# Kernel tuning notes

Hardware: AMD Instinct MI355X
Metric: run time of the kernel (lower is better)

The kernel has to match this reference:

```python
import jax, jax.numpy as jnp
import numpy as np

def setup_inputs() -> dict:
    key = jax.random.key(0)
    k1, k2, k3 = jax.random.split(key, 3)
    shape = (2, 2048, 8, 64)  # [n, l, h, d]
    return {
        "q": jax.random.normal(k1, shape, dtype=jnp.float32),
        "k": jax.random.normal(k2, shape, dtype=jnp.float32),
        "v": jax.random.normal(k3, shape, dtype=jnp.float32),
    }

def reference(q, k, v):
    # QK^T: [n, l, s, h]
    qk = jnp.einsum('nlhd,nshd->nlsh', q, k)
    softmax_temp = 1.0 / (q.shape[3] ** 0.5)
    attn = jax.nn.softmax(softmax_temp * qk, axis=2)
    # weighted values: [n, l, h, d]
    return jnp.einsum('nlsh,nshd->nlhd', attn, v)
```

## Files before the change

kernel.cpp:

```cpp
#include <hip/hip_runtime.h>
#include <hip/hip_bf16.h>
#include <math.h>

typedef float floatx16 __attribute__((ext_vector_type(16)));
typedef __bf16 bf16x8 __attribute__((ext_vector_type(8)));

#define SEQ 2048
#define NH 8
#define DH 64
#define HEADS 16
#define HSTRIDE (SEQ * DH)
#define TILE_E (64 * 64)
#define SLOT_B 32768

__device__ __forceinline__ unsigned short f2bf(float x) {
  union { __bf16 b; unsigned short u; } c; c.b = (__bf16)x; return c.u;
}
__device__ __forceinline__ unsigned int pk2bf(float a, float b) {
  union { __hip_bfloat162 h2; unsigned int u; } c;
  c.h2 = __float22bfloat162_rn(make_float2(a, b));
  return c.u;
}

__device__ __forceinline__ void hswap_fwd(unsigned& a, unsigned& b) {
  asm volatile("v_permlane32_swap_b32 %0, %1" : "+v"(a), "+v"(b));
}
__device__ __forceinline__ void hswap_rev(unsigned& a, unsigned& b) {
  asm volatile("v_permlane32_swap_b32 %0, %1" : "+v"(b), "+v"(a));
}

__device__ __forceinline__ void lds_dma16(const void* g, void* l) {
  __builtin_amdgcn_global_load_lds(
      (const __attribute__((address_space(1))) void*)g,
      (__attribute__((address_space(3))) void*)l, 16, 0, 0);
}

__global__ __launch_bounds__(256)
void pack_kv(const float* __restrict__ k, const float* __restrict__ v,
             unsigned short* __restrict__ kb, unsigned short* __restrict__ vb) {
  __shared__ unsigned short Ts[64][68];
  const int tid  = threadIdx.x;
  const int bx   = blockIdx.x;
  const int head = bx & 15;
  const int kt   = bx >> 4;
  const int n = head >> 3, h = head & 7;

  #pragma unroll
  for (int j2 = 0; j2 < 2; ++j2) {
    int c = j2 * 256 + tid;
    int lane = c & 63;
    int kk = (c >> 6) & 3, ks2 = c >> 8;
    int row = kt * 64 + ks2 * 32 + (lane & 31);
    int d0  = kk * 16 + (lane >> 5) * 8;
    const float* src = k + ((size_t)(n * SEQ + row) * NH + h) * DH + d0;
    float4 a = *(const float4*)src;
    float4 b = *(const float4*)(src + 4);
    ushort4 lo, hi;
    lo.x = f2bf(a.x); lo.y = f2bf(a.y); lo.z = f2bf(a.z); lo.w = f2bf(a.w);
    hi.x = f2bf(b.x); hi.y = f2bf(b.y); hi.z = f2bf(b.z); hi.w = f2bf(b.w);
    unsigned short* dst = kb + (size_t)head * HSTRIDE + kt * TILE_E + c * 8;
    *(ushort4*)dst = lo;
    *(ushort4*)(dst + 4) = hi;
  }

  #pragma unroll
  for (int i = 0; i < 4; ++i) {
    int id = i * 256 + tid;
    int s  = id >> 4;
    int c4 = (id & 15) * 4;
    size_t g = ((size_t)((n * SEQ + kt * 64 + s) * NH + h)) * DH + c4;
    float4 x = *(const float4*)(v + g);
    ushort4 y;
    y.x = f2bf(x.x); y.y = f2bf(x.y); y.z = f2bf(x.z); y.w = f2bf(x.w);
    *(ushort4*)&Ts[s][c4] = y;
  }
  __syncthreads();
  #pragma unroll
  for (int j2 = 0; j2 < 2; ++j2) {
    int c = j2 * 256 + tid;
    int lane = c & 63;
    int dsub = (c >> 6) & 1, ss = c >> 7;
    int s0 = ss * 16 + (lane >> 5) * 8;
    int d  = dsub * 32 + (lane & 31);
    ushort4 lo, hi;
    lo.x = Ts[s0 + 0][d]; lo.y = Ts[s0 + 1][d]; lo.z = Ts[s0 + 2][d]; lo.w = Ts[s0 + 3][d];
    hi.x = Ts[s0 + 4][d]; hi.y = Ts[s0 + 5][d]; hi.z = Ts[s0 + 6][d]; hi.w = Ts[s0 + 7][d];
    unsigned short* dst = vb + (size_t)head * HSTRIDE + kt * TILE_E + c * 8;
    *(ushort4*)dst = lo;
    *(ushort4*)(dst + 4) = hi;
  }
}

__global__ __launch_bounds__(256)
void attn(const float* __restrict__ q, const unsigned short* __restrict__ kb,
          const unsigned short* __restrict__ vt, float* __restrict__ out) {
  __shared__ __align__(16) char lds[2 * SLOT_B];
  float* oM = (float*)lds;
  float* lM = (float*)(lds + 4 * 16 * 72 * 4);

  const int tid  = threadIdx.x;
  const int wave = tid >> 6;
  const int lane = tid & 63;
  const int l32  = lane & 31;
  const int hl   = lane >> 5;
  const int wq   = wave >> 1;
  const int wk   = wave & 1;

  unsigned px = (unsigned)lane, py = (unsigned)lane + 100u;
  hswap_fwd(px, py);
  const bool mir = (__builtin_amdgcn_readfirstlane(px) != 0u);

  const int bx   = blockIdx.x;
  const int head = bx & 15;
  const int qc   = bx >> 4;
  const int n = head >> 3, h = head & 7;

  const unsigned short* kf = kb + (size_t)head * HSTRIDE;
  const unsigned short* vf = vt + (size_t)head * HSTRIDE;

  auto stage = [&](int i, int slot) {
    const unsigned short* g = ((wave & 1) ? vf : kf)
                            + (size_t)((wave >> 1) * 16 + i) * TILE_E;
    char* lb = lds + slot * SLOT_B + wave * 8192;
    #pragma unroll
    for (int j = 0; j < 8; ++j)
      lds_dma16(g + (j * 64 + lane) * 8, lb + j * 1024);
  };

  const float S = 0.125f * 1.4426950408889634f;

  bf16x8 qB[4];
  #pragma unroll
  for (int kk = 0; kk < 4; ++kk) {
    const int row = qc * 64 + wq * 32 + l32;
    const float* src = q + ((size_t)((n * SEQ + row) * NH + h)) * DH + kk * 16 + hl * 8;
    float4 x0 = *(const float4*)src;
    float4 x1 = *(const float4*)(src + 4);
    union { unsigned int u32[4]; bf16x8 v8; } u;
    u.u32[0] = pk2bf(x0.x * S, x0.y * S); u.u32[1] = pk2bf(x0.z * S, x0.w * S);
    u.u32[2] = pk2bf(x1.x * S, x1.y * S); u.u32[3] = pk2bf(x1.z * S, x1.w * S);
    qB[kk] = u.v8;
  }

  floatx16 o[2];
  float lsum = 0.f;
  #pragma unroll
  for (int d = 0; d < 2; ++d)
    #pragma unroll
    for (int i = 0; i < 16; ++i) o[d][i] = 0.f;

  stage(0, 0);

  for (int it = 0; it < 16; ++it) {
    asm volatile("s_waitcnt vmcnt(0)" ::: "memory");
    __builtin_amdgcn_s_barrier();
    __builtin_amdgcn_sched_barrier(0);
    if (it < 15) stage(it + 1, (it + 1) & 1);

    const char* tb = lds + (it & 1) * SLOT_B + wk * 16384;

    bf16x8 kA0[4], kA1[4];
    bf16x8 vb0[2][2], vb1[2][2];
    #pragma unroll
    for (int kk = 0; kk < 4; ++kk)
      kA0[kk] = *(const bf16x8*)(tb + (kk * 64 + lane) * 16);
    #pragma unroll
    for (int kk = 0; kk < 4; ++kk)
      kA1[kk] = *(const bf16x8*)(tb + ((4 + kk) * 64 + lane) * 16);
    #pragma unroll
    for (int j = 0; j < 2; ++j)
      #pragma unroll
      for (int d = 0; d < 2; ++d) {
        vb0[j][d] = *(const bf16x8*)(tb + 8192 + ((j * 2 + d) * 64 + lane) * 16);
        vb1[j][d] = *(const bf16x8*)(tb + 8192 + (((2 + j) * 2 + d) * 64 + lane) * 16);
      }

    floatx16 acc0;
    #pragma unroll
    for (int i = 0; i < 16; ++i) acc0[i] = 0.f;
    __builtin_amdgcn_s_setprio(1);
    #pragma unroll
    for (int kk = 0; kk < 4; ++kk)
      acc0 = __builtin_amdgcn_mfma_f32_32x32x16_bf16(kA0[kk], qB[kk], acc0, 0, 0, 0);
    __builtin_amdgcn_s_setprio(0);

    unsigned pkv0[8];
    #pragma unroll
    for (int g2 = 0; g2 < 4; ++g2) {
      float p0 = __builtin_amdgcn_exp2f(acc0[4 * g2 + 0]);
      float p1 = __builtin_amdgcn_exp2f(acc0[4 * g2 + 1]);
      float p2 = __builtin_amdgcn_exp2f(acc0[4 * g2 + 2]);
      float p3 = __builtin_amdgcn_exp2f(acc0[4 * g2 + 3]);
      lsum += (p0 + p1) + (p2 + p3);
      pkv0[g2 * 2]     = pk2bf(p0, p1);
      pkv0[g2 * 2 + 1] = pk2bf(p2, p3);
    }

    floatx16 acc1;
    #pragma unroll
    for (int i = 0; i < 16; ++i) acc1[i] = 0.f;
    __builtin_amdgcn_s_setprio(1);
    #pragma unroll
    for (int kk = 0; kk < 4; ++kk)
      acc1 = __builtin_amdgcn_mfma_f32_32x32x16_bf16(kA1[kk], qB[kk], acc1, 0, 0, 0);
    __builtin_amdgcn_s_setprio(0);

    {
      union { unsigned u32[4]; bf16x8 v8; } A1, A2;
      A1.u32[0] = pkv0[0]; A1.u32[2] = pkv0[2];
      A1.u32[1] = pkv0[1]; A1.u32[3] = pkv0[3];
      A2.u32[0] = pkv0[4]; A2.u32[2] = pkv0[6];
      A2.u32[1] = pkv0[5]; A2.u32[3] = pkv0[7];
      if (!mir) {
        hswap_fwd(A1.u32[0], A1.u32[2]); hswap_fwd(A1.u32[1], A1.u32[3]);
        hswap_fwd(A2.u32[0], A2.u32[2]); hswap_fwd(A2.u32[1], A2.u32[3]);
      } else {
        hswap_rev(A1.u32[0], A1.u32[2]); hswap_rev(A1.u32[1], A1.u32[3]);
        hswap_rev(A2.u32[0], A2.u32[2]); hswap_rev(A2.u32[1], A2.u32[3]);
      }
      __builtin_amdgcn_s_setprio(1);
      o[0] = __builtin_amdgcn_mfma_f32_32x32x16_bf16(A1.v8, vb0[0][0], o[0], 0, 0, 0);
      o[1] = __builtin_amdgcn_mfma_f32_32x32x16_bf16(A1.v8, vb0[0][1], o[1], 0, 0, 0);
      o[0] = __builtin_amdgcn_mfma_f32_32x32x16_bf16(A2.v8, vb0[1][0], o[0], 0, 0, 0);
      o[1] = __builtin_amdgcn_mfma_f32_32x32x16_bf16(A2.v8, vb0[1][1], o[1], 0, 0, 0);
      __builtin_amdgcn_s_setprio(0);
    }

    {
      unsigned pkv1[8];
      #pragma unroll
      for (int g2 = 0; g2 < 4; ++g2) {
        float p0 = __builtin_amdgcn_exp2f(acc1[4 * g2 + 0]);
        float p1 = __builtin_amdgcn_exp2f(acc1[4 * g2 + 1]);
        float p2 = __builtin_amdgcn_exp2f(acc1[4 * g2 + 2]);
        float p3 = __builtin_amdgcn_exp2f(acc1[4 * g2 + 3]);
        lsum += (p0 + p1) + (p2 + p3);
        pkv1[g2 * 2]     = pk2bf(p0, p1);
        pkv1[g2 * 2 + 1] = pk2bf(p2, p3);
      }
      union { unsigned u32[4]; bf16x8 v8; } A1, A2;
      A1.u32[0] = pkv1[0]; A1.u32[2] = pkv1[2];
      A1.u32[1] = pkv1[1]; A1.u32[3] = pkv1[3];
      A2.u32[0] = pkv1[4]; A2.u32[2] = pkv1[6];
      A2.u32[1] = pkv1[5]; A2.u32[3] = pkv1[7];
      if (!mir) {
        hswap_fwd(A1.u32[0], A1.u32[2]); hswap_fwd(A1.u32[1], A1.u32[3]);
        hswap_fwd(A2.u32[0], A2.u32[2]); hswap_fwd(A2.u32[1], A2.u32[3]);
      } else {
        hswap_rev(A1.u32[0], A1.u32[2]); hswap_rev(A1.u32[1], A1.u32[3]);
        hswap_rev(A2.u32[0], A2.u32[2]); hswap_rev(A2.u32[1], A2.u32[3]);
      }
      __builtin_amdgcn_s_setprio(1);
      o[0] = __builtin_amdgcn_mfma_f32_32x32x16_bf16(A1.v8, vb1[0][0], o[0], 0, 0, 0);
      o[1] = __builtin_amdgcn_mfma_f32_32x32x16_bf16(A1.v8, vb1[0][1], o[1], 0, 0, 0);
      o[0] = __builtin_amdgcn_mfma_f32_32x32x16_bf16(A2.v8, vb1[1][0], o[0], 0, 0, 0);
      o[1] = __builtin_amdgcn_mfma_f32_32x32x16_bf16(A2.v8, vb1[1][1], o[1], 0, 0, 0);
      __builtin_amdgcn_s_setprio(0);
    }
  }

  lsum += __shfl_xor(lsum, 32, 64);

  const int prow = tid >> 4;
  const int col4 = tid & 15;
  #pragma unroll
  for (int p = 0; p < 4; ++p) {
    const int qsel = p >> 1, rh = p & 1;
    __syncthreads();
    #pragma unroll
    for (int r8 = 0; r8 < 8; ++r8) {
      const int r   = rh * 8 + r8;
      const int rip = (r8 & 3) + 4 * hl + 8 * (r8 >> 2);
      oM[(wave * 16 + rip) * 72 + l32]      = o[0][r];
      oM[(wave * 16 + rip) * 72 + 32 + l32] = o[1][r];
    }
    if (lane < 32 && ((lane >> 4) & 1) == rh) lM[wave * 16 + (lane & 15)] = lsum;
    __syncthreads();
    float4 s = make_float4(0.f, 0.f, 0.f, 0.f);
    float l = 0.f;
    #pragma unroll
    for (int j = 0; j < 2; ++j) {
      const int w = qsel * 2 + j;
      float4 t4 = *(const float4*)&oM[(w * 16 + prow) * 72 + col4 * 4];
      s.x += t4.x; s.y += t4.y; s.z += t4.z; s.w += t4.w;
      l += lM[w * 16 + prow];
    }
    float inv = 1.f / l;
    const int grow = qc * 64 + qsel * 32 + rh * 16 + prow;
    float4 st; st.x = s.x * inv; st.y = s.y * inv; st.z = s.z * inv; st.w = s.w * inv;
    *(float4*)(out + ((size_t)((n * SEQ + grow) * NH + h)) * DH + col4 * 4) = st;
  }
}

extern "C" void kernel_launch(void* const* d_in, const int* in_sizes, int n_in,
                              void* d_out, int out_size, void* d_ws, size_t ws_size,
                              hipStream_t stream) {
  const float* q = (const float*)d_in[0];
  const float* k = (const float*)d_in[1];
  const float* v = (const float*)d_in[2];
  float* out = (float*)d_out;
  (void)in_sizes; (void)n_in; (void)out_size; (void)ws_size;

  unsigned short* kb = (unsigned short*)d_ws;
  unsigned short* vb = kb + (size_t)HEADS * HSTRIDE;

  pack_kv<<<HEADS * (SEQ / 64), 256, 0, stream>>>(k, v, kb, vb);
  attn<<<HEADS * (SEQ / 64), 256, 0, stream>>>(q, kb, vb, out);
}
```

Before: 102.4 us.

## Use 512-thread blocks with 128 query rows and triple-buffered KV staging

```diff
diff --git a/kernel.cpp b/kernel.cpp
--- a/kernel.cpp
+++ b/kernel.cpp
@@ -12,6 +12,7 @@
 #define HSTRIDE (SEQ * DH)
 #define TILE_E (64 * 64)
 #define SLOT_B 32768
+#define NSLOT 3
 
 __device__ __forceinline__ unsigned short f2bf(float x) {
   union { __bf16 b; unsigned short u; } c; c.b = (__bf16)x; return c.u;
@@ -91,12 +92,12 @@
   }
 }
 
-__global__ __launch_bounds__(256)
+__global__ __launch_bounds__(512)
 void attn(const float* __restrict__ q, const unsigned short* __restrict__ kb,
           const unsigned short* __restrict__ vt, float* __restrict__ out) {
-  __shared__ __align__(16) char lds[2 * SLOT_B];
+  extern __shared__ __align__(16) char lds[];
   float* oM = (float*)lds;
-  float* lM = (float*)(lds + 4 * 16 * 72 * 4);
+  float* lM = (float*)(lds + 8 * 16 * 72 * 4);
 
   const int tid  = threadIdx.x;
   const int wave = tid >> 6;
@@ -112,19 +113,23 @@
 
   const int bx   = blockIdx.x;
   const int head = bx & 15;
-  const int qc   = bx >> 4;
+  const int qb   = bx >> 4;
   const int n = head >> 3, h = head & 7;
 
   const unsigned short* kf = kb + (size_t)head * HSTRIDE;
   const unsigned short* vf = vt + (size_t)head * HSTRIDE;
 
   auto stage = [&](int i, int slot) {
-    const unsigned short* g = ((wave & 1) ? vf : kf)
-                            + (size_t)((wave >> 1) * 16 + i) * TILE_E;
-    char* lb = lds + slot * SLOT_B + wave * 8192;
-    #pragma unroll
-    for (int j = 0; j < 8; ++j)
-      lds_dma16(g + (j * 64 + lane) * 8, lb + j * 1024);
+    const int tsel  = wave >> 2;
+    const int kvsel = (wave >> 1) & 1;
+    const int half  = wave & 1;
+    const unsigned short* g = (kvsel ? vf : kf) + (size_t)(tsel * 16 + i) * TILE_E;
+    char* lb = lds + slot * SLOT_B + tsel * 16384 + kvsel * 8192 + half * 4096;
+    #pragma unroll
+    for (int j = 0; j < 4; ++j) {
+      const int frag = half * 4 + j;
+      lds_dma16(g + (frag * 64 + lane) * 8, lb + j * 1024);
+    }
   };
 
   const float S = 0.125f * 1.4426950408889634f;
@@ -132,7 +137,7 @@
   bf16x8 qB[4];
   #pragma unroll
   for (int kk = 0; kk < 4; ++kk) {
-    const int row = qc * 64 + wq * 32 + l32;
+    const int row = qb * 128 + wq * 32 + l32;
     const float* src = q + ((size_t)((n * SEQ + row) * NH + h)) * DH + kk * 16 + hl * 8;
     float4 x0 = *(const float4*)src;
     float4 x1 = *(const float4*)(src + 4);
@@ -149,15 +154,23 @@
     #pragma unroll
     for (int i = 0; i < 16; ++i) o[d][i] = 0.f;
 
+  asm volatile("s_waitcnt vmcnt(0)" ::: "memory");
+  __builtin_amdgcn_sched_barrier(0);
+
   stage(0, 0);
+  stage(1, 1);
 
   for (int it = 0; it < 16; ++it) {
-    asm volatile("s_waitcnt vmcnt(0)" ::: "memory");
+    if (it < 15) asm volatile("s_waitcnt vmcnt(4)" ::: "memory");
+    else         asm volatile("s_waitcnt vmcnt(0)" ::: "memory");
     __builtin_amdgcn_s_barrier();
     __builtin_amdgcn_sched_barrier(0);
-    if (it < 15) stage(it + 1, (it + 1) & 1);
-
-    const char* tb = lds + (it & 1) * SLOT_B + wk * 16384;
+    if (it < 14) {
+      int st = it + 2;
+      stage(st, st - (st / 3) * 3);
+    }
+
+    const char* tb = lds + (it - (it / 3) * 3) * SLOT_B + wk * 16384;
 
     bf16x8 kA0[4], kA1[4];
     bf16x8 vb0[2][2], vb1[2][2];
@@ -261,11 +274,14 @@
 
   lsum += __shfl_xor(lsum, 32, 64);
 
-  const int prow = tid >> 4;
-  const int col4 = tid & 15;
+  const int qsel2 = tid >> 8;
+  const int t8    = tid & 255;
+  const int prow  = t8 >> 4;
+  const int col4  = t8 & 15;
   #pragma unroll
   for (int p = 0; p < 4; ++p) {
-    const int qsel = p >> 1, rh = p & 1;
+    const int rh = p & 1;
+    const int qsel = qsel2 * 2 + (p >> 1);
     __syncthreads();
     #pragma unroll
     for (int r8 = 0; r8 < 8; ++r8) {
@@ -286,7 +302,7 @@
       l += lM[w * 16 + prow];
     }
     float inv = 1.f / l;
-    const int grow = qc * 64 + qsel * 32 + rh * 16 + prow;
+    const int grow = qb * 128 + qsel * 32 + rh * 16 + prow;
     float4 st; st.x = s.x * inv; st.y = s.y * inv; st.z = s.z * inv; st.w = s.w * inv;
     *(float4*)(out + ((size_t)((n * SEQ + grow) * NH + h)) * DH + col4 * 4) = st;
   }
@@ -305,5 +321,5 @@
   unsigned short* vb = kb + (size_t)HEADS * HSTRIDE;
 
   pack_kv<<<HEADS * (SEQ / 64), 256, 0, stream>>>(k, v, kb, vb);
-  attn<<<HEADS * (SEQ / 64), 256, 0, stream>>>(q, kb, vb, out);
-}
+  attn<<<HEADS * (SEQ / 128), 512, NSLOT * SLOT_B, stream>>>(q, kb, vb, out);
+}
```

Measured after the change: 99.95 us. 1.02x faster.
